# Kernel optimization log

Measured on AMD Instinct MI355X. Metric: run time of the kernel, lower is better.

## Reference

```python
import jax, jax.numpy as jnp
import numpy as np

ALPHA = 0.2  # LeakyReLU negative slope
NEG_BIG = -9e15


def setup_inputs() -> dict:
    key = jax.random.key(0)
    k1, k2, k3, k4 = jax.random.split(key, 4)
    B, N, Fin, Fout = 16, 1024, 256, 256
    h = jax.random.normal(k1, (B, N, Fin), dtype=jnp.float32)
    adj = jax.random.randint(k2, (B, N, N), 0, 2, dtype=jnp.int32)
    # xavier_uniform with gain=1.414
    def xavier(k, shape, gain=1.414):
        fan_in, fan_out = shape[0], shape[1]
        bound = gain * np.sqrt(6.0 / (fan_in + fan_out))
        return jax.random.uniform(k, shape, jnp.float32, -bound, bound)
    W = xavier(k3, (Fin, Fout))
    a = xavier(k4, (2 * Fout, 1))
    return {"h": h, "adj": adj, "W": W, "a": a}


def reference(h, adj, W, a):
    # h: [B,N,Fin], adj: [B,N,N], W: [Fin,Fout], a: [2*Fout,1]
    Fout = W.shape[1]
    Wh = jnp.einsum('bnf,fo->bno', h, W)                      # [B,N,Fout]
    a1, a2 = a[:Fout, 0], a[Fout:, 0]                          # [Fout], [Fout]
    # e_ij = leakyrelu(Wh_i . a1 + Wh_j . a2) -- outer sum, no O(N^2*F) tensor
    f1 = Wh @ a1                                               # [B,N]
    f2 = Wh @ a2                                               # [B,N]
    e = jax.nn.leaky_relu(f1[:, :, None] + f2[:, None, :], negative_slope=ALPHA)
    attention = jnp.where(adj > 0, e, jnp.float32(NEG_BIG))    # [B,N,N]
    attention = jax.nn.softmax(attention, axis=2)
    h_prime = jnp.einsum('bij,bjo->bio', attention, Wh)        # [B,N,Fout]
    return jax.nn.elu(h_prime)
```

## Files before the change

### kernel.cpp

```cpp
#include <hip/hip_runtime.h>
#include <hip/hip_bf16.h>

#define Bsz 16
#define Nn  1024
#define Ff  256
#define ALPHA 0.2f
#define NEG_BIG -9.0e15f

typedef __attribute__((ext_vector_type(8))) short short8;
typedef __attribute__((ext_vector_type(4))) float f32x4;
typedef __attribute__((ext_vector_type(4))) unsigned short ushort4_t;

__device__ __forceinline__ unsigned short f2bf(float x) {
    union { __hip_bfloat16 b; unsigned short u; } cv;
    cv.b = __float2bfloat16(x);
    return cv.u;
}

__global__ __launch_bounds__(256) void gat_prep(
    const float* __restrict__ W, const float* __restrict__ a,
    float* __restrict__ w1, float* __restrict__ w2)
{
    const int t = threadIdx.x, w = t >> 6, ln = t & 63;
    __shared__ float a1s[Ff], a2s[Ff];
    a1s[t] = a[t];
    a2s[t] = a[Ff + t];
    __syncthreads();
    const int f = blockIdx.x * 4 + w;
    float s1 = 0.f, s2 = 0.f;
    #pragma unroll
    for (int c = 0; c < 4; c++) {
        const int o = ln + 64 * c;
        const float wv = W[(size_t)f * Ff + o];
        s1 += wv * a1s[o];
        s2 += wv * a2s[o];
    }
    #pragma unroll
    for (int off = 1; off < 64; off <<= 1) {
        s1 += __shfl_xor(s1, off, 64);
        s2 += __shfl_xor(s2, off, 64);
    }
    if (ln == 0) { w1[f] = s1; w2[f] = s2; }
}

__global__ __launch_bounds__(256) void pack_f(
    const float* __restrict__ h, const float* __restrict__ W,
    const float* __restrict__ w1, const float* __restrict__ w2,
    unsigned short* __restrict__ hK, unsigned short* __restrict__ WK,
    float* __restrict__ f1, float* __restrict__ f2)
{
    __shared__ float tile[32][257];
    const int id = blockIdx.x, t = threadIdx.x, w = t >> 6, ln = t & 63;
    const bool isH = (id < 512);
    const float* src;
    unsigned short* dst;
    int grow0 = 0;
    if (isH) {
        const int b = id >> 5, kt = id & 31;
        grow0 = b * Nn + kt * 32;
        src = h + (size_t)grow0 * Ff;
        dst = hK + ((size_t)(b * 32 + kt)) * 8192;
    } else {
        const int ft = id - 512;
        src = W + (size_t)ft * 32 * Ff;
        dst = WK + (size_t)ft * 8192;
    }
    #pragma unroll
    for (int rr = 0; rr < 8; rr++) {
        const int row = rr * 4 + w;
        const int col = ln * 4;
        const float4 v = *(const float4*)&src[row * Ff + col];
        tile[row][col] = v.x; tile[row][col + 1] = v.y;
        tile[row][col + 2] = v.z; tile[row][col + 3] = v.w;
    }
    __syncthreads();

    unsigned* d32 = (unsigned*)dst;
    #pragma unroll
    for (int k = 0; k < 16; k++) {
        const int fidx = k * 256 + t;
        const int o = fidx >> 4, q = fidx & 15;
        const unsigned lo = f2bf(tile[2 * q][o]);
        const unsigned hi = f2bf(tile[2 * q + 1][o]);
        d32[fidx] = lo | (hi << 16);
    }

    if (isH) {
        float w1r[4], w2r[4];
        #pragma unroll
        for (int c = 0; c < 4; c++) {
            w1r[c] = w1[ln + 64 * c];
            w2r[c] = w2[ln + 64 * c];
        }
        #pragma unroll
        for (int rr = 0; rr < 8; rr++) {
            const int row = rr * 4 + w;
            float s1 = 0.f, s2 = 0.f;
            #pragma unroll
            for (int c = 0; c < 4; c++) {
                const float hv = tile[row][ln + 64 * c];
                s1 += hv * w1r[c];
                s2 += hv * w2r[c];
            }
            #pragma unroll
            for (int off = 1; off < 64; off <<= 1) {
                s1 += __shfl_xor(s1, off, 64);
                s2 += __shfl_xor(s2, off, 64);
            }
            if (ln == 0) { f1[grow0 + row] = s1; f2[grow0 + row] = s2; }
        }
    }
}

#define TI 32
__global__ __launch_bounds__(512, 4) void gat_attn(
    const int* __restrict__ adj,
    const float* __restrict__ f1, const float* __restrict__ f2,
    const unsigned short* __restrict__ hK, const unsigned short* __restrict__ WK,
    float* __restrict__ out)
{
    __shared__ unsigned short pbf[TI * 1024];
    const int t = threadIdx.x, w = t >> 6, ln = t & 63;
    const int m = ln & 15, quad = ln >> 4;
    const int bid = blockIdx.x;
    const int b  = 2 * (bid & 7) + ((bid >> 3) & 1);
    const int i0 = (bid >> 4) * TI;

    float4 f2r[4];
    #pragma unroll
    for (int c = 0; c < 4; c++)
        f2r[c] = *(const float4*)&f2[b * Nn + 256 * c + 4 * ln];

    #pragma unroll
    for (int p = 0; p < 2; p++) {
        const int r0 = w * 4 + 2 * p, r1 = r0 + 1;
        const int gr = b * Nn + i0 + r0;
        const int* a0 = adj + (size_t)gr * Nn;
        const int* a1 = a0 + Nn;
        int4 av0[4], av1[4];
        #pragma unroll
        for (int c = 0; c < 4; c++) {
            av0[c] = *(const int4*)&a0[256 * c + 4 * ln];
            av1[c] = *(const int4*)&a1[256 * c + 4 * ln];
        }
        const float fi0 = f1[gr], fi1 = f1[gr + 1];
        float e0[16], e1[16];
        float mx0 = -INFINITY, mx1 = -INFINITY;
        #pragma unroll
        for (int c = 0; c < 4; c++) {
            const float4 fv = f2r[c];
            float x;
            x = fi0 + fv.x; x = x > 0.f ? x : ALPHA * x; x = av0[c].x > 0 ? x : NEG_BIG; e0[4*c+0] = x; mx0 = fmaxf(mx0, x);
            x = fi0 + fv.y; x = x > 0.f ? x : ALPHA * x; x = av0[c].y > 0 ? x : NEG_BIG; e0[4*c+1] = x; mx0 = fmaxf(mx0, x);
            x = fi0 + fv.z; x = x > 0.f ? x : ALPHA * x; x = av0[c].z > 0 ? x : NEG_BIG; e0[4*c+2] = x; mx0 = fmaxf(mx0, x);
            x = fi0 + fv.w; x = x > 0.f ? x : ALPHA * x; x = av0[c].w > 0 ? x : NEG_BIG; e0[4*c+3] = x; mx0 = fmaxf(mx0, x);
            x = fi1 + fv.x; x = x > 0.f ? x : ALPHA * x; x = av1[c].x > 0 ? x : NEG_BIG; e1[4*c+0] = x; mx1 = fmaxf(mx1, x);
            x = fi1 + fv.y; x = x > 0.f ? x : ALPHA * x; x = av1[c].y > 0 ? x : NEG_BIG; e1[4*c+1] = x; mx1 = fmaxf(mx1, x);
            x = fi1 + fv.z; x = x > 0.f ? x : ALPHA * x; x = av1[c].z > 0 ? x : NEG_BIG; e1[4*c+2] = x; mx1 = fmaxf(mx1, x);
            x = fi1 + fv.w; x = x > 0.f ? x : ALPHA * x; x = av1[c].w > 0 ? x : NEG_BIG; e1[4*c+3] = x; mx1 = fmaxf(mx1, x);
        }
        #pragma unroll
        for (int off = 1; off < 64; off <<= 1) {
            mx0 = fmaxf(mx0, __shfl_xor(mx0, off, 64));
            mx1 = fmaxf(mx1, __shfl_xor(mx1, off, 64));
        }
        float s0 = 0.f, s1 = 0.f;
        #pragma unroll
        for (int c = 0; c < 16; c++) {
            e0[c] = __expf(e0[c] - mx0); s0 += e0[c];
            e1[c] = __expf(e1[c] - mx1); s1 += e1[c];
        }
        #pragma unroll
        for (int off = 1; off < 64; off <<= 1) {
            s0 += __shfl_xor(s0, off, 64);
            s1 += __shfl_xor(s1, off, 64);
        }
        const float ri0 = 1.f / s0, ri1 = 1.f / s1;
        #pragma unroll
        for (int c = 0; c < 4; c++) {
            const int j = 256 * c + 4 * ln;
            ushort4_t v0 = { f2bf(e0[4*c] * ri0), f2bf(e0[4*c+1] * ri0),
                             f2bf(e0[4*c+2] * ri0), f2bf(e0[4*c+3] * ri0) };
            ushort4_t v1 = { f2bf(e1[4*c] * ri1), f2bf(e1[4*c+1] * ri1),
                             f2bf(e1[4*c+2] * ri1), f2bf(e1[4*c+3] * ri1) };
            *(ushort4_t*)&pbf[r0 * 1024 + (j ^ ((r0 & 7) << 3))] = v0;
            *(ushort4_t*)&pbf[r1 * 1024 + (j ^ ((r1 & 7) << 3))] = v1;
        }
    }
    __syncthreads();

    const int mt = w & 1, n0 = (w >> 1) << 6;
    const unsigned short* hKb = hK + (size_t)b * 32 * 8192;
    const int arow = (mt * 16 + m) * 1024;
    const int asw  = (m & 7) << 3;
    f32x4 acc[4] = {{0.f,0.f,0.f,0.f},{0.f,0.f,0.f,0.f},{0.f,0.f,0.f,0.f},{0.f,0.f,0.f,0.f}};

    short8 afc = *(const short8*)&pbf[arow + ((quad * 8) ^ asw)];
    short8 bc[4];
    #pragma unroll
    for (int nt = 0; nt < 4; nt++)
        bc[nt] = *(const short8*)&hKb[(n0 + nt * 16 + m) * 32 + quad * 8];
    for (int kt = 0; kt < 31; kt++) {
        const short8 afn = *(const short8*)&pbf[arow + (((kt + 1) * 32 + quad * 8) ^ asw)];
        short8 bn[4];
        #pragma unroll
        for (int nt = 0; nt < 4; nt++)
            bn[nt] = *(const short8*)&hKb[(size_t)(kt + 1) * 8192 + (n0 + nt * 16 + m) * 32 + quad * 8];
        #pragma unroll
        for (int nt = 0; nt < 4; nt++)
            acc[nt] = __builtin_amdgcn_mfma_f32_16x16x32_bf16(afc, bc[nt], acc[nt], 0, 0, 0);
        afc = afn;
        #pragma unroll
        for (int nt = 0; nt < 4; nt++) bc[nt] = bn[nt];
    }
    #pragma unroll
    for (int nt = 0; nt < 4; nt++)
        acc[nt] = __builtin_amdgcn_mfma_f32_16x16x32_bf16(afc, bc[nt], acc[nt], 0, 0, 0);

    __syncthreads();
    #pragma unroll
    for (int nt = 0; nt < 4; nt++)
        #pragma unroll
        for (int reg = 0; reg < 4; reg++)
            pbf[(mt * 16 + quad * 4 + reg) * 264 + n0 + nt * 16 + m] = f2bf(acc[nt][reg]);
    __syncthreads();

    f32x4 acc2[4] = {{0.f,0.f,0.f,0.f},{0.f,0.f,0.f,0.f},{0.f,0.f,0.f,0.f},{0.f,0.f,0.f,0.f}};
    #pragma unroll
    for (int kt = 0; kt < 8; kt++) {
        const short8 af = *(const short8*)&pbf[(mt * 16 + m) * 264 + kt * 32 + quad * 8];
        #pragma unroll
        for (int nt = 0; nt < 4; nt++) {
            const short8 bv = *(const short8*)&WK[(size_t)kt * 8192 + (n0 + nt * 16 + m) * 32 + quad * 8];
            acc2[nt] = __builtin_amdgcn_mfma_f32_16x16x32_bf16(af, bv, acc2[nt], 0, 0, 0);
        }
    }
    #pragma unroll
    for (int nt = 0; nt < 4; nt++) {
        #pragma unroll
        for (int reg = 0; reg < 4; reg++) {
            const int row = mt * 16 + quad * 4 + reg;
            const int col = n0 + nt * 16 + m;
            float v = acc2[nt][reg];
            v = (v > 0.f) ? v : (__expf(v) - 1.0f);
            out[((size_t)(b * Nn) + i0 + row) * Ff + col] = v;
        }
    }
}

extern "C" void kernel_launch(void* const* d_in, const int* in_sizes, int n_in,
                              void* d_out, int out_size, void* d_ws, size_t ws_size,
                              hipStream_t stream)
{
    const void* h   = d_in[0];
    const void* adj = d_in[1];
    const void* W   = d_in[2];
    const void* a   = d_in[3];
    for (int i = 0; i < n_in; i++) {
        if      (in_sizes[i] == Bsz * Nn * Ff) h   = d_in[i];
        else if (in_sizes[i] == Bsz * Nn * Nn) adj = d_in[i];
        else if (in_sizes[i] == Ff * Ff)       W   = d_in[i];
        else if (in_sizes[i] == 2 * Ff)        a   = d_in[i];
    }
    float* out = (float*)d_out;

    char*  wsb = (char*)d_ws;
    float* w1  = (float*)wsb;
    float* w2  = w1 + Ff;
    float* f1  = (float*)(wsb + 4096);
    float* f2  = f1 + Bsz * Nn;
    unsigned short* hK = (unsigned short*)(wsb + 4096 + 2 * 65536);
    unsigned short* WK = hK + (size_t)Bsz * 32 * 8192;

    gat_prep<<<64, 256, 0, stream>>>((const float*)W, (const float*)a, w1, w2);
    pack_f<<<520, 256, 0, stream>>>((const float*)h, (const float*)W, w1, w2, hK, WK, f1, f2);
    gat_attn<<<Bsz * (Nn / TI), 512, 0, stream>>>((const int*)adj, f1, f2, hK, WK, out);
}
```

Baseline: 158.1 us.

## Retile attention MFMA to 2x2 per wave and prefetch adjacency rows

Each wave now computes a 32x32 output tile as 2x2 MFMA blocks instead of a 16x64 strip. This halves the global hK/WK fragment loads per wave and reuses both A and B fragments across two MFMAs. The hK loads get a two-step-ahead prefetch, the k-loop is fully unrolled, and the second adjacency row pair is loaded before the first pair's softmax to hide global latency. In exchange, register pressure rises under the 512-thread, 4-block launch bound, which risks spills or lower occupancy.

Result: faster. 142.7 us (-9.7%).

```diff
diff --git a/kernel.cpp b/kernel.cpp
--- a/kernel.cpp
+++ b/kernel.cpp
@@ -131,19 +131,26 @@
     for (int c = 0; c < 4; c++)
         f2r[c] = *(const float4*)&f2[b * Nn + 256 * c + 4 * ln];
 
+    const int grb = b * Nn + i0 + w * 4;
+    const int* aptr = adj + (size_t)grb * Nn;
+    int4 av0[4], av1[4];
+    #pragma unroll
+    for (int c = 0; c < 4; c++) {
+        av0[c] = *(const int4*)&aptr[c * 256 + 4 * ln];
+        av1[c] = *(const int4*)&aptr[Nn + c * 256 + 4 * ln];
+    }
     #pragma unroll
     for (int p = 0; p < 2; p++) {
+        int4 nv0[4], nv1[4];
+        if (p == 0) {
+            #pragma unroll
+            for (int c = 0; c < 4; c++) {
+                nv0[c] = *(const int4*)&aptr[2 * Nn + c * 256 + 4 * ln];
+                nv1[c] = *(const int4*)&aptr[3 * Nn + c * 256 + 4 * ln];
+            }
+        }
         const int r0 = w * 4 + 2 * p, r1 = r0 + 1;
-        const int gr = b * Nn + i0 + r0;
-        const int* a0 = adj + (size_t)gr * Nn;
-        const int* a1 = a0 + Nn;
-        int4 av0[4], av1[4];
-        #pragma unroll
-        for (int c = 0; c < 4; c++) {
-            av0[c] = *(const int4*)&a0[256 * c + 4 * ln];
-            av1[c] = *(const int4*)&a1[256 * c + 4 * ln];
-        }
-        const float fi0 = f1[gr], fi1 = f1[gr + 1];
+        const float fi0 = f1[grb + 2 * p], fi1 = f1[grb + 2 * p + 1];
         float e0[16], e1[16];
         float mx0 = -INFINITY, mx1 = -INFINITY;
         #pragma unroll
@@ -186,65 +193,76 @@
             *(ushort4_t*)&pbf[r0 * 1024 + (j ^ ((r0 & 7) << 3))] = v0;
             *(ushort4_t*)&pbf[r1 * 1024 + (j ^ ((r1 & 7) << 3))] = v1;
         }
-    }
-    __syncthreads();
-
-    const int mt = w & 1, n0 = (w >> 1) << 6;
+        #pragma unroll
+        for (int c = 0; c < 4; c++) { av0[c] = nv0[c]; av1[c] = nv1[c]; }
+    }
+    __syncthreads();
+
+    const int n0 = w * 32;
     const unsigned short* hKb = hK + (size_t)b * 32 * 8192;
-    const int arow = (mt * 16 + m) * 1024;
-    const int asw  = (m & 7) << 3;
-    f32x4 acc[4] = {{0.f,0.f,0.f,0.f},{0.f,0.f,0.f,0.f},{0.f,0.f,0.f,0.f},{0.f,0.f,0.f,0.f}};
-
-    short8 afc = *(const short8*)&pbf[arow + ((quad * 8) ^ asw)];
-    short8 bc[4];
-    #pragma unroll
-    for (int nt = 0; nt < 4; nt++)
-        bc[nt] = *(const short8*)&hKb[(n0 + nt * 16 + m) * 32 + quad * 8];
-    for (int kt = 0; kt < 31; kt++) {
-        const short8 afn = *(const short8*)&pbf[arow + (((kt + 1) * 32 + quad * 8) ^ asw)];
-        short8 bn[4];
-        #pragma unroll
-        for (int nt = 0; nt < 4; nt++)
-            bn[nt] = *(const short8*)&hKb[(size_t)(kt + 1) * 8192 + (n0 + nt * 16 + m) * 32 + quad * 8];
-        #pragma unroll
-        for (int nt = 0; nt < 4; nt++)
-            acc[nt] = __builtin_amdgcn_mfma_f32_16x16x32_bf16(afc, bc[nt], acc[nt], 0, 0, 0);
-        afc = afn;
-        #pragma unroll
-        for (int nt = 0; nt < 4; nt++) bc[nt] = bn[nt];
-    }
-    #pragma unroll
-    for (int nt = 0; nt < 4; nt++)
-        acc[nt] = __builtin_amdgcn_mfma_f32_16x16x32_bf16(afc, bc[nt], acc[nt], 0, 0, 0);
-
-    __syncthreads();
-    #pragma unroll
-    for (int nt = 0; nt < 4; nt++)
-        #pragma unroll
-        for (int reg = 0; reg < 4; reg++)
-            pbf[(mt * 16 + quad * 4 + reg) * 264 + n0 + nt * 16 + m] = f2bf(acc[nt][reg]);
-    __syncthreads();
-
-    f32x4 acc2[4] = {{0.f,0.f,0.f,0.f},{0.f,0.f,0.f,0.f},{0.f,0.f,0.f,0.f},{0.f,0.f,0.f,0.f}};
+    const int arow0 = m * 1024, arow1 = (16 + m) * 1024;
+    const int asw = (m & 7) << 3;
+    #define AF0(kt) (*(const short8*)&pbf[arow0 + ((((kt) * 32) + quad * 8) ^ asw)])
+    #define AF1(kt) (*(const short8*)&pbf[arow1 + ((((kt) * 32) + quad * 8) ^ asw)])
+    #define BF0(kt) (*(const short8*)&hKb[(size_t)(kt) * 8192 + (n0 + m) * 32 + quad * 8])
+    #define BF1(kt) (*(const short8*)&hKb[(size_t)(kt) * 8192 + (n0 + 16 + m) * 32 + quad * 8])
+
+    f32x4 acc00 = {0.f,0.f,0.f,0.f}, acc01 = acc00, acc10 = acc00, acc11 = acc00;
+    short8 a0c = AF0(0), a1c = AF1(0);
+    short8 b0c = BF0(0), b1c = BF1(0);
+    short8 b0n = BF0(1), b1n = BF1(1);
+    #pragma unroll
+    for (int kt = 0; kt < 32; kt++) {
+        short8 b0nn = b0c, b1nn = b1c, a0n = a0c, a1n = a1c;
+        if (kt + 2 < 32) { b0nn = BF0(kt + 2); b1nn = BF1(kt + 2); }
+        if (kt + 1 < 32) { a0n = AF0(kt + 1); a1n = AF1(kt + 1); }
+        acc00 = __builtin_amdgcn_mfma_f32_16x16x32_bf16(a0c, b0c, acc00, 0, 0, 0);
+        acc01 = __builtin_amdgcn_mfma_f32_16x16x32_bf16(a0c, b1c, acc01, 0, 0, 0);
+        acc10 = __builtin_amdgcn_mfma_f32_16x16x32_bf16(a1c, b0c, acc10, 0, 0, 0);
+        acc11 = __builtin_amdgcn_mfma_f32_16x16x32_bf16(a1c, b1c, acc11, 0, 0, 0);
+        a0c = a0n; a1c = a1n; b0c = b0n; b1c = b1n; b0n = b0nn; b1n = b1nn;
+    }
+
+    __syncthreads();
+    #pragma unroll
+    for (int reg = 0; reg < 4; reg++) {
+        pbf[(quad * 4 + reg) * 264 + n0 + m]           = f2bf(acc00[reg]);
+        pbf[(quad * 4 + reg) * 264 + n0 + 16 + m]      = f2bf(acc01[reg]);
+        pbf[(16 + quad * 4 + reg) * 264 + n0 + m]      = f2bf(acc10[reg]);
+        pbf[(16 + quad * 4 + reg) * 264 + n0 + 16 + m] = f2bf(acc11[reg]);
+    }
+    __syncthreads();
+
+    #define GA0(kt) (*(const short8*)&pbf[m * 264 + (kt) * 32 + quad * 8])
+    #define GA1(kt) (*(const short8*)&pbf[(16 + m) * 264 + (kt) * 32 + quad * 8])
+    #define WB0(kt) (*(const short8*)&WK[(size_t)(kt) * 8192 + (n0 + m) * 32 + quad * 8])
+    #define WB1(kt) (*(const short8*)&WK[(size_t)(kt) * 8192 + (n0 + 16 + m) * 32 + quad * 8])
+
+    f32x4 c00 = {0.f,0.f,0.f,0.f}, c01 = c00, c10 = c00, c11 = c00;
+    short8 ga0 = GA0(0), ga1 = GA1(0);
+    short8 wb0 = WB0(0), wb1 = WB1(0);
     #pragma unroll
     for (int kt = 0; kt < 8; kt++) {
-        const short8 af = *(const short8*)&pbf[(mt * 16 + m) * 264 + kt * 32 + quad * 8];
-        #pragma unroll
-        for (int nt = 0; nt < 4; nt++) {
-            const short8 bv = *(const short8*)&WK[(size_t)kt * 8192 + (n0 + nt * 16 + m) * 32 + quad * 8];
-            acc2[nt] = __builtin_amdgcn_mfma_f32_16x16x32_bf16(af, bv, acc2[nt], 0, 0, 0);
-        }
-    }
-    #pragma unroll
-    for (int nt = 0; nt < 4; nt++) {
-        #pragma unroll
-        for (int reg = 0; reg < 4; reg++) {
-            const int row = mt * 16 + quad * 4 + reg;
-            const int col = n0 + nt * 16 + m;
-            float v = acc2[nt][reg];
-            v = (v > 0.f) ? v : (__expf(v) - 1.0f);
-            out[((size_t)(b * Nn) + i0 + row) * Ff + col] = v;
-        }
+        short8 ga0n = ga0, ga1n = ga1, wb0n = wb0, wb1n = wb1;
+        if (kt + 1 < 8) { ga0n = GA0(kt+1); ga1n = GA1(kt+1); wb0n = WB0(kt+1); wb1n = WB1(kt+1); }
+        c00 = __builtin_amdgcn_mfma_f32_16x16x32_bf16(ga0, wb0, c00, 0, 0, 0);
+        c01 = __builtin_amdgcn_mfma_f32_16x16x32_bf16(ga0, wb1, c01, 0, 0, 0);
+        c10 = __builtin_amdgcn_mfma_f32_16x16x32_bf16(ga1, wb0, c10, 0, 0, 0);
+        c11 = __builtin_amdgcn_mfma_f32_16x16x32_bf16(ga1, wb1, c11, 0, 0, 0);
+        ga0 = ga0n; ga1 = ga1n; wb0 = wb0n; wb1 = wb1n;
+    }
+    const size_t ob = (size_t)(b * Nn) + i0;
+    #pragma unroll
+    for (int reg = 0; reg < 4; reg++) {
+        float v;
+        v = c00[reg]; v = v > 0.f ? v : (__expf(v) - 1.f);
+        out[(ob + quad * 4 + reg) * Ff + n0 + m] = v;
+        v = c01[reg]; v = v > 0.f ? v : (__expf(v) - 1.f);
+        out[(ob + quad * 4 + reg) * Ff + n0 + 16 + m] = v;
+        v = c10[reg]; v = v > 0.f ? v : (__expf(v) - 1.f);
+        out[(ob + 16 + quad * 4 + reg) * Ff + n0 + m] = v;
+        v = c11[reg]; v = v > 0.f ? v : (__expf(v) - 1.f);
+        out[(ob + 16 + quad * 4 + reg) * Ff + n0 + 16 + m] = v;
     }
 }
 
```
